# Optimization experiments

Measured on AMD Instinct MI355X. Metric: run time of the kernel, lower is better.

## Reference

```python
import jax, jax.numpy as jnp
import numpy as np

N = 2048   # nodes
E = 8      # edge types (num_edge)
C = 8      # channels (num_channels)


def setup_inputs() -> dict:
    key = jax.random.key(0)
    k0, k1, k2, k3, k4 = jax.random.split(key, 5)
    # adjacency stack [1, N, N, E]; non-negative like adjacency weights
    A = jax.random.uniform(k0, (1, N, N, E), dtype=jnp.float32)
    # GTConv weights [out_channels, in_channels, 1, 1]
    w1_0 = jax.random.normal(k1, (C, E, 1, 1), dtype=jnp.float32) * 0.1
    w2_0 = jax.random.normal(k2, (C, E, 1, 1), dtype=jnp.float32) * 0.1
    w_1 = jax.random.normal(k3, (C, E, 1, 1), dtype=jnp.float32) * 0.1
    w_2 = jax.random.normal(k4, (C, E, 1, 1), dtype=jnp.float32) * 0.1
    return {"A": A, "w1_0": w1_0, "w2_0": w2_0, "w_1": w_1, "w_2": w_2}


def _gtconv(Ap, w):
    # Ap: [1, E, N, N]; w: [C, E, 1, 1] -> softmax over edge-type dim, mix, sum
    sw = jax.nn.softmax(w, axis=1)           # [C, E, 1, 1]
    return jnp.sum(Ap * sw, axis=1)          # [C, N, N]


def _normalize(H):
    # Per channel: zero diagonal, then scale column j by 1/sum_i H[i,j]
    # (equivalent to torch code's transpose -> row degree norm -> transpose)
    n = H.shape[-1]
    Hm = H * (1.0 - jnp.eye(n, dtype=H.dtype))[None]   # [C, N, N] diag zeroed
    deg = jnp.sum(Hm, axis=1)                           # [C, N] column sums
    deg_safe = jnp.where(deg == 0, jnp.ones_like(deg), deg)
    deg_inv = jnp.where(deg == 0, jnp.zeros_like(deg), 1.0 / deg_safe)
    return Hm * deg_inv[:, None, :]


def reference(A, w1_0, w2_0, w_1, w_2):
    Ap = jnp.transpose(A, (0, 3, 1, 2))      # [1, E, N, N]
    a = _gtconv(Ap, w1_0)                    # [C, N, N]
    b = _gtconv(Ap, w2_0)                    # [C, N, N]
    H = jnp.matmul(a, b)                     # batched meta-path product
    for w in (w_1, w_2):
        H = _normalize(H)
        H = jnp.matmul(H, _gtconv(Ap, w))
    Hm = jnp.mean(H, axis=0)                 # [N, N]
    return (Hm + Hm.T) * 0.5
```

## Files before the change

kernel.cpp:

```cpp
#include <hip/hip_runtime.h>
#include <hip/hip_bf16.h>

using short8 = __attribute__((ext_vector_type(8))) short;
using f32x4  = __attribute__((ext_vector_type(4))) float;

#define NN 2048
#define NC 8
static const size_t PLANE = (size_t)NN * NN;

__device__ __forceinline__ void gload16(const void* g, void* l) {
  __builtin_amdgcn_global_load_lds((const __attribute__((address_space(1))) unsigned int*)g,
                                   (__attribute__((address_space(3))) unsigned int*)l, 16, 0, 0);
}

__global__ __launch_bounds__(256) void softmax_w_k(const float* __restrict__ w0, const float* __restrict__ w1,
                                                   const float* __restrict__ w2, const float* __restrict__ w3,
                                                   float* __restrict__ sw) {
  int t = threadIdx.x;
  const float* srcs[4] = {w0, w1, w2, w3};
  float v = srcs[t >> 6][t & 63];
  float m = v;
  #pragma unroll
  for (int d = 1; d < 8; d <<= 1) m = fmaxf(m, __shfl_xor(m, d, 8));
  float ex = __expf(v - m);
  float s = ex;
  #pragma unroll
  for (int d = 1; d < 8; d <<= 1) s += __shfl_xor(s, d, 8);
  sw[t] = ex / s;
}

template<int W4>
__global__ __launch_bounds__(512) void gtconv_fused(const float* __restrict__ A, const float* __restrict__ sw,
                                                    short* __restrict__ a, short* __restrict__ bT,
                                                    short* __restrict__ c1T, short* __restrict__ c2T) {
  __shared__ float tile[16384];
  __shared__ float swl[256];
  const int t = threadIdx.x;
  const int i0 = blockIdx.y * 32, j0 = blockIdx.x * 64;
  if (t < 256) swl[t] = sw[t];

  const float* Abase = A + ((size_t)i0 * NN + j0) * 8;
  #pragma unroll
  for (int q = 0; q < 8; q++) {
    const int d = q * 512 + t;
    const int s = (d & ~15) | ((d ^ (d >> 4)) & 15);
    const int row = s >> 7, fc = s & 127;
    gload16(Abase + (size_t)row * (NN * 8) + fc * 4, &tile[(q * 512 + (t & ~63)) * 4]);
  }
  asm volatile("s_waitcnt vmcnt(0)" ::: "memory");
  __syncthreads();

  {
    const int ch = t & 1, jg = (t >> 1) & 7, ii = t >> 4;
    const int sxx = (ii * 8 + jg) & 15;
    const int fb = ii * 128 + jg * 16;
    float acc[4][8];
    #pragma unroll
    for (int cc = 0; cc < 4; cc++)
      #pragma unroll
      for (int p = 0; p < 8; p++) acc[cc][p] = 0.f;
    #pragma unroll
    for (int p = 0; p < 8; p++) {
      const int k0 = p * 2;
      const float4 v0 = *reinterpret_cast<const float4*>(&tile[((fb & ~15) | (k0 ^ sxx)) * 4]);
      const float4 v1 = *reinterpret_cast<const float4*>(&tile[((fb & ~15) | ((k0 + 1) ^ sxx)) * 4]);
      const float e[8] = {v0.x, v0.y, v0.z, v0.w, v1.x, v1.y, v1.z, v1.w};
      #pragma unroll
      for (int cc = 0; cc < 4; cc++) {
        const int c = ch * 4 + cc;
        #pragma unroll
        for (int k = 0; k < 8; k++) acc[cc][p] += e[k] * swl[c * 8 + k];
      }
    }
    #pragma unroll
    for (int cc = 0; cc < 4; cc++) {
      const int c = ch * 4 + cc;
      short8 o;
      #pragma unroll
      for (int p = 0; p < 8; p++) {
        __hip_bfloat16 hb = __float2bfloat16(acc[cc][p]);
        o[p] = *reinterpret_cast<short*>(&hb);
      }
      *reinterpret_cast<short8*>(a + (size_t)c * PLANE + (size_t)(i0 + ii) * NN + j0 + jg * 8) = o;
    }
  }

  {
    const int ch = t & 1, ig = (t >> 1) & 3, jj = t >> 3;
    const int NT_OUT = W4 ? 3 : 2;
    short* outs[3] = {bT, c1T, c2T};
    #pragma unroll
    for (int T = 0; T < NT_OUT; T++) {
      short* outp = outs[T];
      const float* swt = &swl[(T + 1) * 64];
      float acc[4][8];
      #pragma unroll
      for (int cc = 0; cc < 4; cc++)
        #pragma unroll
        for (int p = 0; p < 8; p++) acc[cc][p] = 0.f;
      #pragma unroll
      for (int p = 0; p < 8; p++) {
        const int irow = ig * 8 + p;
        const int fb = irow * 128 + jj * 2;
        const int sxx = (irow * 8 + (jj >> 3)) & 15;
        const int k0 = fb & 15;
        const float4 v0 = *reinterpret_cast<const float4*>(&tile[((fb & ~15) | (k0 ^ sxx)) * 4]);
        const float4 v1 = *reinterpret_cast<const float4*>(&tile[((fb & ~15) | ((k0 + 1) ^ sxx)) * 4]);
        const float e[8] = {v0.x, v0.y, v0.z, v0.w, v1.x, v1.y, v1.z, v1.w};
        #pragma unroll
        for (int cc = 0; cc < 4; cc++) {
          const int c = ch * 4 + cc;
          #pragma unroll
          for (int k = 0; k < 8; k++) acc[cc][p] += e[k] * swt[c * 8 + k];
        }
      }
      #pragma unroll
      for (int cc = 0; cc < 4; cc++) {
        const int c = ch * 4 + cc;
        short8 o;
        #pragma unroll
        for (int p = 0; p < 8; p++) {
          __hip_bfloat16 hb = __float2bfloat16(acc[cc][p]);
          o[p] = *reinterpret_cast<short*>(&hb);
        }
        *reinterpret_cast<short8*>(outp + (size_t)c * PLANE + (size_t)(j0 + jj) * NN + i0 + ig * 8) = o;
      }
    }
  }
}

__global__ __launch_bounds__(256) void gtconv_one(const float* __restrict__ A, const float* __restrict__ sw,
                                                  __hip_bfloat16* __restrict__ oT) {
  __shared__ float Als[32][33][9];
  __shared__ float swl[8][8];
  int t = threadIdx.x;
  if (t < 64) swl[t >> 3][t & 7] = sw[t];
  int i0 = blockIdx.y * 32, j0 = blockIdx.x * 32;
  #pragma unroll
  for (int q = 0; q < 8; q++) {
    int fi = t + q * 256;
    int e4 = fi & 1, jj = (fi >> 1) & 31, ii = fi >> 6;
    const float4 v = *reinterpret_cast<const float4*>(A + (((size_t)(i0 + ii) * NN + (j0 + jj)) << 3) + e4 * 4);
    float* dst = &Als[ii][jj][e4 * 4];
    dst[0] = v.x; dst[1] = v.y; dst[2] = v.z; dst[3] = v.w;
  }
  __syncthreads();
  #pragma unroll
  for (int q = 0; q < 4; q++) {
    int pos = t + q * 256;
    int r = pos >> 5, s = pos & 31;
    float e[8];
    #pragma unroll
    for (int k = 0; k < 8; k++) e[k] = Als[s][r][k];
    size_t base = (size_t)(j0 + r) * NN + (i0 + s);
    #pragma unroll
    for (int c = 0; c < 8; c++) {
      float v1 = 0.f;
      #pragma unroll
      for (int k = 0; k < 8; k++) v1 += e[k] * swl[c][k];
      oT[(size_t)c * PLANE + base] = __float2bfloat16(v1);
    }
  }
}

#define GBM 256
#define GBK 64
template<int CPB, int PARTIALS>
__global__ __launch_bounds__(512, 2) void gemm8(const short* __restrict__ Ag0, const short* __restrict__ Bg0,
                                                float* __restrict__ C, float* __restrict__ degp) {
  __shared__ short lds[65536];
  __shared__ float colred[2][256];
  const int t = threadIdx.x;
  const int lane = t & 63, w = t >> 6;
  const int wr = w >> 2, wc = w & 3;
  const int m0 = blockIdx.y * GBM, n0 = blockIdx.x * GBM;
  const short* Abase = Ag0 + (size_t)blockIdx.z * CPB * PLANE;
  const short* Bbase = Bg0 + (size_t)blockIdx.z * CPB * PLANE;
  const int NT = CPB * 32;

  const int lrow = t >> 3;
  const int lk8  = t & 7;
  const int fr = lane & 15, fk = (lane >> 4) * 8;

  f32x4 acc[8][4] = {};

  auto STAGE = [&](int tt, int p) {
    const int k0 = (tt & 31) * GBK;
    const short* Ag = Abase + (size_t)(tt >> 5) * PLANE;
    const short* Bg = Bbase + (size_t)(tt >> 5) * PLANE;
    #pragma unroll
    for (int q = 0; q < 4; q++) {
      const int row = q * 64 + lrow;
      const int ksrc = ((lk8 ^ (row & 7)) * 8);
      short* la = &lds[p * 32768 +         q * 4096 + w * 512];
      short* lb = &lds[p * 32768 + 16384 + q * 4096 + w * 512];
      gload16(Ag + (size_t)(m0 + row) * NN + k0 + ksrc, la);
      gload16(Bg + (size_t)(n0 + row) * NN + k0 + ksrc, lb);
    }
  };

  STAGE(0, 0);
  STAGE(1, 1);
  asm volatile("s_waitcnt vmcnt(8)" ::: "memory");
  __builtin_amdgcn_sched_barrier(0);
  __builtin_amdgcn_s_barrier();
  __builtin_amdgcn_sched_barrier(0);

  short8 aq[8][2], bq0[2][2], bq1[2][2];

#define LOAD_AQ(PA)                                                                        \
  { _Pragma("unroll") for (int m = 0; m < 8; m++) {                                        \
      const int row = wr * 128 + m * 16 + fr;                                              \
      const int sw8 = (row & 7) * 8;                                                       \
      _Pragma("unroll") for (int kx = 0; kx < 2; kx++)                                     \
        aq[m][kx] = *reinterpret_cast<const short8*>(&(PA)[row * 64 + ((kx * 32 + fk) ^ sw8)]); } }

#define LOAD_BQ(DST, NH, PB)                                                               \
  { _Pragma("unroll") for (int n = 0; n < 2; n++) {                                        \
      const int row = wc * 64 + ((NH) * 2 + n) * 16 + fr;                                  \
      const int sw8 = (row & 7) * 8;                                                       \
      _Pragma("unroll") for (int kx = 0; kx < 2; kx++)                                     \
        DST[n][kx] = *reinterpret_cast<const short8*>(&(PB)[row * 64 + ((kx * 32 + fk) ^ sw8)]); } }

  {
    const short* pA0 = &lds[0];
    const short* pB0 = &lds[16384];
    LOAD_AQ(pA0);
    LOAD_BQ(bq0, 0, pB0);
  }

  for (int tt = 0; tt < NT; ++tt) {
    const int p = tt & 1;
    const short* pB = &lds[p * 32768 + 16384];
    const short* pAn = &lds[(p ^ 1) * 32768];
    const short* pBn = &lds[(p ^ 1) * 32768 + 16384];

    LOAD_BQ(bq1, 1, pB);
    __builtin_amdgcn_sched_barrier(0);

    __builtin_amdgcn_s_setprio(1);
    #pragma unroll
    for (int kx = 0; kx < 2; kx++)
      #pragma unroll
      for (int m = 0; m < 8; m++)
        #pragma unroll
        for (int n = 0; n < 2; n++)
          acc[m][n] = __builtin_amdgcn_mfma_f32_16x16x32_bf16(aq[m][kx], bq0[n][kx], acc[m][n], 0, 0, 0);
    __builtin_amdgcn_s_setprio(0);
    __builtin_amdgcn_sched_barrier(0);

    if (tt + 1 < NT) {
      LOAD_AQ(pAn);
      LOAD_BQ(bq0, 0, pBn);
    }
    __builtin_amdgcn_sched_barrier(0);

    __builtin_amdgcn_s_setprio(1);
    #pragma unroll
    for (int kx = 0; kx < 2; kx++)
      #pragma unroll
      for (int m = 0; m < 8; m++)
        #pragma unroll
        for (int n = 0; n < 2; n++)
          acc[m][n + 2] = __builtin_amdgcn_mfma_f32_16x16x32_bf16(aq[m][kx], bq1[n][kx], acc[m][n + 2], 0, 0, 0);
    __builtin_amdgcn_s_setprio(0);
    __builtin_amdgcn_sched_barrier(0);

    __builtin_amdgcn_s_barrier();
    __builtin_amdgcn_sched_barrier(0);
    if (tt + 2 < NT) {
      STAGE(tt + 2, p);
      asm volatile("s_waitcnt vmcnt(8)" ::: "memory");
    } else {
      asm volatile("s_waitcnt vmcnt(0)" ::: "memory");
    }
    __builtin_amdgcn_sched_barrier(0);
    __builtin_amdgcn_s_barrier();
    __builtin_amdgcn_sched_barrier(0);
  }
#undef LOAD_AQ
#undef LOAD_BQ

  float* Cg = C + (size_t)blockIdx.z * PLANE;
  const int orow = (lane >> 4) * 4, ocol = lane & 15;
  #pragma unroll
  for (int m = 0; m < 8; m++)
    #pragma unroll
    for (int n = 0; n < 4; n++) {
      const int gr = m0 + wr * 128 + m * 16 + orow;
      const int gc = n0 + wc * 64 + n * 16 + ocol;
      #pragma unroll
      for (int j = 0; j < 4; j++)
        Cg[(size_t)(gr + j) * NN + gc] = acc[m][n][j];
    }

  if (PARTIALS) {
    #pragma unroll
    for (int n = 0; n < 4; n++) {
      float s = 0.f;
      #pragma unroll
      for (int m = 0; m < 8; m++)
        #pragma unroll
        for (int j = 0; j < 4; j++) s += acc[m][n][j];
      s += __shfl_xor(s, 16);
      s += __shfl_xor(s, 32);
      if (lane < 16) colred[wr][wc * 64 + n * 16 + lane] = s;
    }
    __syncthreads();
    if (t < 256) {
      float s = colred[0][t] + colred[1][t];
      degp[((size_t)blockIdx.z * 8 + blockIdx.y) * NN + n0 + t] = s;
    }
  }
}

__global__ __launch_bounds__(256) void reduce_inv(const float* __restrict__ degp, const float* __restrict__ H,
                                                  float* __restrict__ deginv) {
  int idx = blockIdx.x * 256 + threadIdx.x;
  int c = idx >> 11, j = idx & (NN - 1);
  float s = 0.f;
  #pragma unroll
  for (int tb = 0; tb < 8; tb++) s += degp[((size_t)c * 8 + tb) * NN + j];
  s -= H[(size_t)c * PLANE + (size_t)j * NN + j];
  deginv[idx] = (s == 0.f) ? 0.f : 1.f / s;
}

__global__ __launch_bounds__(256) void normalize_cast(const float* __restrict__ H, const float* __restrict__ deginv,
                                                      short* __restrict__ Hn) {
  size_t idx = (size_t)blockIdx.x * 256 + threadIdx.x;
  size_t e0 = idx * 8;
  int c = (int)(e0 >> 22);
  size_t rem = e0 & (PLANE - 1);
  int i = (int)(rem >> 11), j0 = (int)(rem & (NN - 1));
  const float4 h0 = *reinterpret_cast<const float4*>(H + e0);
  const float4 h1 = *reinterpret_cast<const float4*>(H + e0 + 4);
  const float4 d0 = *reinterpret_cast<const float4*>(deginv + c * NN + j0);
  const float4 d1 = *reinterpret_cast<const float4*>(deginv + c * NN + j0 + 4);
  float v[8] = {h0.x * d0.x, h0.y * d0.y, h0.z * d0.z, h0.w * d0.w,
                h1.x * d1.x, h1.y * d1.y, h1.z * d1.z, h1.w * d1.w};
  int dd = i - j0;
  if (dd >= 0 && dd < 8) v[dd] = 0.f;
  short8 o;
  #pragma unroll
  for (int k = 0; k < 8; k++) {
    __hip_bfloat16 hb = __float2bfloat16(v[k]);
    o[k] = *reinterpret_cast<short*>(&hb);
  }
  *reinterpret_cast<short8*>(Hn + e0) = o;
}

__global__ __launch_bounds__(256) void final_sym4(const float* __restrict__ M, float* __restrict__ out) {
  __shared__ float tl[64][65];
  int t = threadIdx.x;
  int i0 = blockIdx.y * 64, j0 = blockIdx.x * 64;
  int r0 = t >> 6, cl = t & 63;
  float acc[16];
  #pragma unroll
  for (int q = 0; q < 16; q++) acc[q] = 0.f;
  for (int p = 0; p < 4; p++) {
    const float* Mp = M + (size_t)p * PLANE;
    __syncthreads();
    #pragma unroll
    for (int q = 0; q < 16; q++) {
      int rr = r0 + q * 4;
      tl[rr][cl] = Mp[(size_t)(j0 + rr) * NN + i0 + cl];
    }
    __syncthreads();
    #pragma unroll
    for (int q = 0; q < 16; q++) {
      int rr = r0 + q * 4;
      acc[q] += Mp[(size_t)(i0 + rr) * NN + j0 + cl] + tl[cl][rr];
    }
  }
  #pragma unroll
  for (int q = 0; q < 16; q++) {
    int rr = r0 + q * 4;
    out[(size_t)(i0 + rr) * NN + j0 + cl] = acc[q] * (1.0f / 16.0f);
  }
}

extern "C" void kernel_launch(void* const* d_in, const int* in_sizes, int n_in,
                              void* d_out, int out_size, void* d_ws, size_t ws_size,
                              hipStream_t stream) {
  const float* A    = (const float*)d_in[0];
  const float* w1_0 = (const float*)d_in[1];
  const float* w2_0 = (const float*)d_in[2];
  const float* w_1  = (const float*)d_in[3];
  const float* w_2  = (const float*)d_in[4];
  float* out = (float*)d_out;

  char* w = (char*)d_ws;
  float* sw     = (float*)w;
  float* degp   = (float*)(w + (1 << 17));
  float* deginv = (float*)(w + (1 << 17) + (1 << 21));
  const size_t BSZ = (size_t)NC * PLANE * sizeof(short);
  short* B0 = (short*)(w + (4u << 20));
  short* B1 = (short*)((char*)B0 + BSZ);
  short* B2 = (short*)((char*)B1 + BSZ);
  const size_t HSZ = (size_t)NC * PLANE * sizeof(float);
  const size_t need4 = (4u << 20) + 4 * BSZ + HSZ;
  const bool fused4 = ws_size >= need4;
  short* B3 = (short*)((char*)B2 + BSZ);
  float* HH = fused4 ? (float*)((char*)B3 + BSZ) : (float*)((char*)B2 + BSZ);

  dim3 blk(256), blkg(512);
  dim3 gfuse(NN / 64, NN / 32);
  dim3 gconv(64, 64);
  dim3 ggemm(8, 8, 8);
  dim3 ggemm4(8, 8, 4);

  softmax_w_k<<<1, blk, 0, stream>>>(w1_0, w2_0, w_1, w_2, sw);
  if (fused4) {
    gtconv_fused<1><<<gfuse, blkg, 0, stream>>>(A, sw, B0, B1, B2, B3);
  } else {
    gtconv_fused<0><<<gfuse, blkg, 0, stream>>>(A, sw, B0, B1, B2, B3);
  }

  gemm8<1, 1><<<ggemm, blkg, 0, stream>>>(B0, B1, HH, degp);
  reduce_inv<<<64, blk, 0, stream>>>(degp, HH, deginv);
  normalize_cast<<<16384, blk, 0, stream>>>(HH, deginv, B0);
  if (!fused4) {
    gtconv_one<<<gconv, blk, 0, stream>>>(A, sw + 192, (__hip_bfloat16*)B1);
  }

  gemm8<1, 1><<<ggemm, blkg, 0, stream>>>(B0, B2, HH, degp);
  reduce_inv<<<64, blk, 0, stream>>>(degp, HH, deginv);
  normalize_cast<<<16384, blk, 0, stream>>>(HH, deginv, B0);

  short* Bc2 = fused4 ? B3 : B1;
  gemm8<2, 0><<<ggemm4, blkg, 0, stream>>>(B0, Bc2, HH, degp);
  final_sym4<<<dim3(32, 32), blk, 0, stream>>>(HH, out);
}
```

Before: 645.4 us.

## Replace double-buffered GEMM pipeline with single-buffer loop and split final GEMM per channel

The GEMM mainloop drops the two-stage LDS double buffering and the interleaved fragment prefetch. Each k-step now loads the tile, waits for all loads, reads its fragments and runs all MFMAs in one pass. LDS use is halved, which may allow more resident blocks. The last GEMM now computes one channel per block with 8 output planes, and the symmetrisation kernel sums all 8. This gives up load/compute overlap and adds output traffic in exchange for simpler code and possibly higher occupancy.

```diff
diff --git a/kernel.cpp b/kernel.cpp
--- a/kernel.cpp
+++ b/kernel.cpp
@@ -168,7 +168,7 @@
 template<int CPB, int PARTIALS>
 __global__ __launch_bounds__(512, 2) void gemm8(const short* __restrict__ Ag0, const short* __restrict__ Bg0,
                                                 float* __restrict__ C, float* __restrict__ degp) {
-  __shared__ short lds[65536];
+  __shared__ short lds[32768];
   __shared__ float colred[2][256];
   const int t = threadIdx.x;
   const int lane = t & 63, w = t >> 6;
@@ -184,7 +184,7 @@
 
   f32x4 acc[8][4] = {};
 
-  auto STAGE = [&](int tt, int p) {
+  auto STAGE = [&](int tt) {
     const int k0 = (tt & 31) * GBK;
     const short* Ag = Abase + (size_t)(tt >> 5) * PLANE;
     const short* Bg = Bbase + (size_t)(tt >> 5) * PLANE;
@@ -192,94 +192,52 @@
     for (int q = 0; q < 4; q++) {
       const int row = q * 64 + lrow;
       const int ksrc = ((lk8 ^ (row & 7)) * 8);
-      short* la = &lds[p * 32768 +         q * 4096 + w * 512];
-      short* lb = &lds[p * 32768 + 16384 + q * 4096 + w * 512];
+      short* la = &lds[q * 4096 + w * 512];
+      short* lb = &lds[16384 + q * 4096 + w * 512];
       gload16(Ag + (size_t)(m0 + row) * NN + k0 + ksrc, la);
       gload16(Bg + (size_t)(n0 + row) * NN + k0 + ksrc, lb);
     }
   };
 
-  STAGE(0, 0);
-  STAGE(1, 1);
-  asm volatile("s_waitcnt vmcnt(8)" ::: "memory");
-  __builtin_amdgcn_sched_barrier(0);
-  __builtin_amdgcn_s_barrier();
-  __builtin_amdgcn_sched_barrier(0);
-
-  short8 aq[8][2], bq0[2][2], bq1[2][2];
-
-#define LOAD_AQ(PA)                                                                        \
-  { _Pragma("unroll") for (int m = 0; m < 8; m++) {                                        \
-      const int row = wr * 128 + m * 16 + fr;                                              \
-      const int sw8 = (row & 7) * 8;                                                       \
-      _Pragma("unroll") for (int kx = 0; kx < 2; kx++)                                     \
-        aq[m][kx] = *reinterpret_cast<const short8*>(&(PA)[row * 64 + ((kx * 32 + fk) ^ sw8)]); } }
-
-#define LOAD_BQ(DST, NH, PB)                                                               \
-  { _Pragma("unroll") for (int n = 0; n < 2; n++) {                                        \
-      const int row = wc * 64 + ((NH) * 2 + n) * 16 + fr;                                  \
-      const int sw8 = (row & 7) * 8;                                                       \
-      _Pragma("unroll") for (int kx = 0; kx < 2; kx++)                                     \
-        DST[n][kx] = *reinterpret_cast<const short8*>(&(PB)[row * 64 + ((kx * 32 + fk) ^ sw8)]); } }
-
-  {
-    const short* pA0 = &lds[0];
-    const short* pB0 = &lds[16384];
-    LOAD_AQ(pA0);
-    LOAD_BQ(bq0, 0, pB0);
-  }
+  short8 aq[8][2], bq[4][2];
 
   for (int tt = 0; tt < NT; ++tt) {
-    const int p = tt & 1;
-    const short* pB = &lds[p * 32768 + 16384];
-    const short* pAn = &lds[(p ^ 1) * 32768];
-    const short* pBn = &lds[(p ^ 1) * 32768 + 16384];
-
-    LOAD_BQ(bq1, 1, pB);
-    __builtin_amdgcn_sched_barrier(0);
-
+    STAGE(tt);
+    asm volatile("s_waitcnt vmcnt(0)" ::: "memory");
+    __builtin_amdgcn_sched_barrier(0);
+    __builtin_amdgcn_s_barrier();
+    __builtin_amdgcn_sched_barrier(0);
+
+    #pragma unroll
+    for (int m = 0; m < 8; m++) {
+      const int row = wr * 128 + m * 16 + fr;
+      const int sw8 = (row & 7) * 8;
+      #pragma unroll
+      for (int kx = 0; kx < 2; kx++)
+        aq[m][kx] = *reinterpret_cast<const short8*>(&lds[row * 64 + ((kx * 32 + fk) ^ sw8)]);
+    }
+    #pragma unroll
+    for (int n = 0; n < 4; n++) {
+      const int row = wc * 64 + n * 16 + fr;
+      const int sw8 = (row & 7) * 8;
+      #pragma unroll
+      for (int kx = 0; kx < 2; kx++)
+        bq[n][kx] = *reinterpret_cast<const short8*>(&lds[16384 + row * 64 + ((kx * 32 + fk) ^ sw8)]);
+    }
+    __builtin_amdgcn_sched_barrier(0);
     __builtin_amdgcn_s_setprio(1);
     #pragma unroll
     for (int kx = 0; kx < 2; kx++)
       #pragma unroll
       for (int m = 0; m < 8; m++)
         #pragma unroll
-        for (int n = 0; n < 2; n++)
-          acc[m][n] = __builtin_amdgcn_mfma_f32_16x16x32_bf16(aq[m][kx], bq0[n][kx], acc[m][n], 0, 0, 0);
+        for (int n = 0; n < 4; n++)
+          acc[m][n] = __builtin_amdgcn_mfma_f32_16x16x32_bf16(aq[m][kx], bq[n][kx], acc[m][n], 0, 0, 0);
     __builtin_amdgcn_s_setprio(0);
     __builtin_amdgcn_sched_barrier(0);
-
-    if (tt + 1 < NT) {
-      LOAD_AQ(pAn);
-      LOAD_BQ(bq0, 0, pBn);
-    }
-    __builtin_amdgcn_sched_barrier(0);
-
-    __builtin_amdgcn_s_setprio(1);
-    #pragma unroll
-    for (int kx = 0; kx < 2; kx++)
-      #pragma unroll
-      for (int m = 0; m < 8; m++)
-        #pragma unroll
-        for (int n = 0; n < 2; n++)
-          acc[m][n + 2] = __builtin_amdgcn_mfma_f32_16x16x32_bf16(aq[m][kx], bq1[n][kx], acc[m][n + 2], 0, 0, 0);
-    __builtin_amdgcn_s_setprio(0);
-    __builtin_amdgcn_sched_barrier(0);
-
     __builtin_amdgcn_s_barrier();
     __builtin_amdgcn_sched_barrier(0);
-    if (tt + 2 < NT) {
-      STAGE(tt + 2, p);
-      asm volatile("s_waitcnt vmcnt(8)" ::: "memory");
-    } else {
-      asm volatile("s_waitcnt vmcnt(0)" ::: "memory");
-    }
-    __builtin_amdgcn_sched_barrier(0);
-    __builtin_amdgcn_s_barrier();
-    __builtin_amdgcn_sched_barrier(0);
-  }
-#undef LOAD_AQ
-#undef LOAD_BQ
+  }
 
   float* Cg = C + (size_t)blockIdx.z * PLANE;
   const int orow = (lane >> 4) * 4, ocol = lane & 15;
@@ -349,7 +307,7 @@
   *reinterpret_cast<short8*>(Hn + e0) = o;
 }
 
-__global__ __launch_bounds__(256) void final_sym4(const float* __restrict__ M, float* __restrict__ out) {
+__global__ __launch_bounds__(256) void final_sym8(const float* __restrict__ M, float* __restrict__ out) {
   __shared__ float tl[64][65];
   int t = threadIdx.x;
   int i0 = blockIdx.y * 64, j0 = blockIdx.x * 64;
@@ -357,7 +315,7 @@
   float acc[16];
   #pragma unroll
   for (int q = 0; q < 16; q++) acc[q] = 0.f;
-  for (int p = 0; p < 4; p++) {
+  for (int p = 0; p < 8; p++) {
     const float* Mp = M + (size_t)p * PLANE;
     __syncthreads();
     #pragma unroll
@@ -407,7 +365,6 @@
   dim3 gfuse(NN / 64, NN / 32);
   dim3 gconv(64, 64);
   dim3 ggemm(8, 8, 8);
-  dim3 ggemm4(8, 8, 4);
 
   softmax_w_k<<<1, blk, 0, stream>>>(w1_0, w2_0, w_1, w_2, sw);
   if (fused4) {
@@ -428,6 +385,6 @@
   normalize_cast<<<16384, blk, 0, stream>>>(HH, deginv, B0);
 
   short* Bc2 = fused4 ? B3 : B1;
-  gemm8<2, 0><<<ggemm4, blkg, 0, stream>>>(B0, Bc2, HH, degp);
-  final_sym4<<<dim3(32, 32), blk, 0, stream>>>(HH, out);
-}
+  gemm8<1, 0><<<ggemm, blkg, 0, stream>>>(B0, Bc2, HH, degp);
+  final_sym8<<<dim3(32, 32), blk, 0, stream>>>(HH, out);
+}
```

Result: slower. 792.0 us (+22.7%).
